# Kernel tuning notes

Hardware: AMD Instinct MI355X
Metric: run time of the kernel (lower is better)

## Reference

```python
import jax, jax.numpy as jnp
import numpy as np

N_HEADS, D_MODEL, DK, DV = 16, 1024, 64, 64
B, S = 4, 2048
NEG = -1000000000.0


def setup_inputs() -> dict:
    key = jax.random.key(0)
    ks = jax.random.split(key, 10)
    inp = {
        "q": jax.random.normal(ks[0], (B, S, D_MODEL), jnp.float32),
        "k": jax.random.normal(ks[1], (B, S, D_MODEL), jnp.float32),
        "v": jax.random.normal(ks[2], (B, S, D_MODEL), jnp.float32),
        "padding_mask": jax.random.randint(ks[3], (B, 1, S), 0, 2, jnp.int32),
        # linear params (torch Linear: y = x @ W.T + b); store as [in, out]
        "w_q": jax.random.normal(ks[4], (D_MODEL, N_HEADS * DK), jnp.float32) * 0.02,
        "b_q": jnp.zeros((N_HEADS * DK,), jnp.float32),
        "w_k": jax.random.normal(ks[5], (D_MODEL, N_HEADS * DK), jnp.float32) * 0.02,
        "b_k": jnp.zeros((N_HEADS * DK,), jnp.float32),
        "w_v": jax.random.normal(ks[6], (D_MODEL, N_HEADS * DV), jnp.float32) * 0.02,
        "b_v": jnp.zeros((N_HEADS * DV,), jnp.float32),
    }
    return inp


def reference(q, k, v, padding_mask, w_q, b_q, w_k, b_k, w_v, b_v):
    residual = q
    # project and split heads: [B, H, S, dk]
    qh = (q @ w_q + b_q).reshape(B, S, N_HEADS, DK).transpose(0, 2, 1, 3)
    kh = (k @ w_k + b_k).reshape(B, S, N_HEADS, DK).transpose(0, 2, 1, 3)
    vh = (v @ w_v + b_v).reshape(B, S, N_HEADS, DV).transpose(0, 2, 1, 3)
    # NB: original code DIVIDES by factor = dk**-0.5, i.e. multiplies by sqrt(dk)
    scores = jnp.einsum("bhqd,bhkd->bhqk", qh, kh) / (DK ** -0.5)
    mask = padding_mask[:, None, :, :]  # [B,1,1,S] broadcasts over heads/queries
    scores = jnp.where(mask == 0, NEG, scores)
    attn = jax.nn.softmax(scores, axis=-1)  # dropout = identity (eval)
    ctx = jnp.einsum("bhqk,bhkd->bhqd", attn, vh)
    ctx = ctx.transpose(0, 2, 1, 3).reshape(B, S, N_HEADS * DV)
    return ctx + residual
```

## Files before the change

kernel.cpp:

```cpp
#include <hip/hip_runtime.h>
#include <hip/hip_fp16.h>

#define BB 4
#define SS 2048
#define HH 16
#define DKK 64
#define DMODEL 1024

typedef __attribute__((ext_vector_type(8))) _Float16 half8;
typedef __attribute__((ext_vector_type(4))) _Float16 half4;
typedef __attribute__((ext_vector_type(2))) __fp16 fp16x2;
typedef __attribute__((ext_vector_type(4))) float floatx4;

#define MFMA16(a, b, c) __builtin_amdgcn_mfma_f32_16x16x32_f16(a, b, c, 0, 0, 0)

#define SCL2 11.5415603336f

__device__ __forceinline__ void gload_lds16(const _Float16* g, _Float16* l) {
    __builtin_amdgcn_global_load_lds(
        (const __attribute__((address_space(1))) void*)g,
        (__attribute__((address_space(3))) void*)l, 16, 0, 0);
}

__device__ __forceinline__
void convert_x_body(const float* __restrict__ src, _Float16* __restrict__ dst,
                    int bidx)
{
    size_t base = ((size_t)bidx * 256 + threadIdx.x) * 8;
    int m = (int)(base >> 10);
    int kk = (int)(base & 1023);
    float4 a = *(const float4*)(src + base);
    float4 b = *(const float4*)(src + base + 4);
    half8 h;
    h[0] = (_Float16)a.x; h[1] = (_Float16)a.y; h[2] = (_Float16)a.z; h[3] = (_Float16)a.w;
    h[4] = (_Float16)b.x; h[5] = (_Float16)b.y; h[6] = (_Float16)b.z; h[7] = (_Float16)b.w;
    int kd = kk ^ ((m & 7) << 3);
    *(half8*)(dst + ((size_t)m << 10) + kd) = h;
}

__device__ __forceinline__
void convert_wt_body(const float* __restrict__ W, _Float16* __restrict__ WT,
                     int bidx)
{
    __shared__ __attribute__((aligned(16))) _Float16 T[64][72];
    int kt = (bidx >> 4) << 6;
    int nt = (bidx & 15) << 6;
    int tid = threadIdx.x;
    #pragma unroll
    for (int p = 0; p < 4; p++) {
        int lin = tid + p * 256;
        int row = lin >> 4;
        int c4 = (lin & 15) << 2;
        float4 vv = *(const float4*)(W + (size_t)(kt + row) * DMODEL + nt + c4);
        T[c4 + 0][row] = (_Float16)vv.x;
        T[c4 + 1][row] = (_Float16)vv.y;
        T[c4 + 2][row] = (_Float16)vv.z;
        T[c4 + 3][row] = (_Float16)vv.w;
    }
    __syncthreads();
    #pragma unroll
    for (int p = 0; p < 2; p++) {
        int lin = tid + p * 256;
        int nl = lin >> 3;
        int u = lin & 7;
        half8 h = *(const half8*)&T[nl][u * 8];
        int n = nt + nl;
        int kd = kt + ((u ^ (n & 7)) << 3);
        *(half8*)(WT + (size_t)n * DMODEL + kd) = h;
    }
}

__global__ __launch_bounds__(256)
void convert_x(const float* __restrict__ q, const float* __restrict__ k,
               const float* __restrict__ v, _Float16* __restrict__ xq,
               _Float16* __restrict__ xk, _Float16* __restrict__ xv)
{
    int z = blockIdx.y;
    convert_x_body(z == 0 ? q : z == 1 ? k : v,
                   z == 0 ? xq : z == 1 ? xk : xv, blockIdx.x);
}

__global__ __launch_bounds__(256)
void convert_wt(const float* __restrict__ wq, const float* __restrict__ wk,
                const float* __restrict__ wv, _Float16* __restrict__ tq,
                _Float16* __restrict__ tk, _Float16* __restrict__ tv)
{
    int z = blockIdx.y;
    convert_wt_body(z == 0 ? wq : z == 1 ? wk : wv,
                    z == 0 ? tq : z == 1 ? tk : tv, blockIdx.x);
}

__global__ __launch_bounds__(256)
void convert_all(const float* __restrict__ q, const float* __restrict__ k,
                 const float* __restrict__ v, const float* __restrict__ wq,
                 const float* __restrict__ wk, const float* __restrict__ wv,
                 _Float16* __restrict__ xq, _Float16* __restrict__ xk,
                 _Float16* __restrict__ xv, _Float16* __restrict__ tq,
                 _Float16* __restrict__ tk, _Float16* __restrict__ tv)
{
    int y = blockIdx.y;
    if (y < 3) {
        convert_x_body(y == 0 ? q : y == 1 ? k : v,
                       y == 0 ? xq : y == 1 ? xk : xv, blockIdx.x);
    } else {
        if (blockIdx.x >= 768) return;
        int z = blockIdx.x >> 8;
        convert_wt_body(z == 0 ? wq : z == 1 ? wk : wv,
                        z == 0 ? tq : z == 1 ? tk : tv, blockIdx.x & 255);
    }
}

template <int VMODE, int SWZ>
__device__ __forceinline__
void proj_body(const _Float16* __restrict__ X, const _Float16* __restrict__ WT,
               const float* __restrict__ bias, _Float16* __restrict__ out,
               int bidx, float scl)
{
    __shared__ __attribute__((aligned(16))) _Float16 As[128 * 64];
    __shared__ __attribute__((aligned(16))) _Float16 Bs[128 * 64];
    const int tid = threadIdx.x;
    const int wave = tid >> 6, lane = tid & 63, quad = lane >> 4, l16 = lane & 15;
    const int wm = wave >> 1, wn = wave & 1;
    const int m0 = ((bidx & 7) | ((bidx >> 6) << 3)) << 7;
    const int n0 = ((bidx >> 3) & 7) << 7;
    const int lrow = lane >> 3;
    const int lcol = (lane & 7) << 3;

    floatx4 acc[4][4] = {};

    for (int k0 = 0; k0 < DMODEL; k0 += 64) {
        __syncthreads();
        #pragma unroll
        for (int c = 0; c < 4; c++) {
            int row = c * 32 + wave * 8;
            gload_lds16(X + (size_t)(m0 + row + lrow) * DMODEL + k0 + lcol,
                        As + (size_t)row * 64);
            gload_lds16(WT + (size_t)(n0 + row + lrow) * DMODEL + k0 + lcol,
                        Bs + (size_t)row * 64);
        }
        __syncthreads();
        #pragma unroll
        for (int ks = 0; ks < 2; ks++) {
            int ccol = ((ks * 4 + quad) ^ (l16 & 7)) << 3;
            half8 af[4], bf[4];
            #pragma unroll
            for (int i = 0; i < 4; i++)
                af[i] = *(const half8*)(As + (wm * 64 + i * 16 + l16) * 64 + ccol);
            #pragma unroll
            for (int j = 0; j < 4; j++)
                bf[j] = *(const half8*)(Bs + (wn * 64 + j * 16 + l16) * 64 + ccol);
            #pragma unroll
            for (int i = 0; i < 4; i++)
                #pragma unroll
                for (int j = 0; j < 4; j++)
                    acc[i][j] = VMODE ? MFMA16(bf[j], af[i], acc[i][j])
                                      : MFMA16(af[i], bf[j], acc[i][j]);
        }
    }

    if (VMODE == 0) {
        #pragma unroll
        for (int j = 0; j < 4; j++) {
            int ng = n0 + wn * 64 + j * 16 + l16;
            int h = ng >> 6, d = ng & 63;
            float bv = bias[ng];
            #pragma unroll
            for (int i = 0; i < 4; i++)
                #pragma unroll
                for (int r = 0; r < 4; r++) {
                    int mg = m0 + wm * 64 + i * 16 + quad * 4 + r;
                    int bb = mg >> 11, s = mg & 2047;
                    int dd = SWZ ? ((((d >> 3) ^ (s & 7)) << 3) | (d & 7)) : d;
                    out[(((size_t)bb * HH + h) * SS + s) * DKK + dd] =
                        (_Float16)((acc[i][j][r] + bv) * scl);
                }
        }
    } else {
        #pragma unroll
        for (int j = 0; j < 4; j++)
            #pragma unroll
            for (int r = 0; r < 4; r++) {
                int ng = n0 + wn * 64 + j * 16 + quad * 4 + r;
                int h = ng >> 6, d = ng & 63;
                float bv = bias[ng];
                #pragma unroll
                for (int i = 0; i < 4; i++) {
                    int mg = m0 + wm * 64 + i * 16 + l16;
                    int bb = mg >> 11, s = mg & 2047;
                    int ss2 = SWZ ? (s ^ ((d & 7) << 3)) : s;
                    out[(((size_t)bb * HH + h) * DKK + d) * SS + ss2] =
                        (_Float16)((acc[i][j][r] + bv) * scl);
                }
            }
    }
}

template <int VMODE, int SWZ>
__global__ __launch_bounds__(256)
void proj128(const _Float16* __restrict__ X, const _Float16* __restrict__ WT,
             const float* __restrict__ bias, _Float16* __restrict__ out, float scl)
{
    proj_body<VMODE, SWZ>(X, WT, bias, out, blockIdx.x, scl);
}

__global__ __launch_bounds__(256)
void proj_all(const _Float16* __restrict__ Xq, const _Float16* __restrict__ Xk,
              const _Float16* __restrict__ Xv, const _Float16* __restrict__ WTq,
              const _Float16* __restrict__ WTk, const _Float16* __restrict__ WTv,
              const float* __restrict__ bq, const float* __restrict__ bk,
              const float* __restrict__ bv, _Float16* __restrict__ Qh,
              _Float16* __restrict__ Kh, _Float16* __restrict__ VTh)
{
    int z = blockIdx.y;
    if (z == 0)      proj_body<0, 0>(Xq, WTq, bq, Qh, blockIdx.x, SCL2);
    else if (z == 1) proj_body<0, 1>(Xk, WTk, bk, Kh, blockIdx.x, 1.0f);
    else             proj_body<1, 1>(Xv, WTv, bv, VTh, blockIdx.x, 1.0f);
}

__global__ __launch_bounds__(256)
void flash3(const _Float16* __restrict__ Qw, const _Float16* __restrict__ Kw,
            const _Float16* __restrict__ VTw, const int* __restrict__ mask,
            const float* __restrict__ resid, float* __restrict__ out)
{
    __shared__ float Bias[SS];
    __shared__ __attribute__((aligned(16))) _Float16 Plds[4][2][16][64];
    __shared__ __attribute__((aligned(16))) _Float16 Ks[2][4096];
    __shared__ __attribute__((aligned(16))) _Float16 Vs[2][4096];

    const int tid = threadIdx.x;
    const int wave = tid >> 6, lane = tid & 63, quad = lane >> 4, l16 = lane & 15;
    const int bx = blockIdx.x;
    const int xcd = bx & 7;
    const int jj = bx >> 3;
    const int bh = ((jj >> 4) << 3) | xcd;
    const int qt = jj & 15;
    const int b = bh >> 4;
    const int h = bh & 15;
    const int qbase = qt * 128 + wave * 32;
    const int sw = l16 & 7;

    const _Float16* Kbase = Kw + (size_t)bh * SS * DKK;
    const _Float16* Vbase = VTw + (size_t)bh * DKK * SS;

    half8 qf[2][2];
    #pragma unroll
    for (int mt = 0; mt < 2; mt++) {
        const _Float16* Qp = Qw + ((size_t)bh * SS + qbase + mt * 16 + l16) * DKK;
        qf[mt][0] = *(const half8*)(Qp + quad * 8);
        qf[mt][1] = *(const half8*)(Qp + 32 + quad * 8);
    }

    #pragma unroll
    for (int c = 0; c < 2; c++) {
        int chunk = wave * 2 + c;
        gload_lds16(Kbase + chunk * 512 + lane * 8, &Ks[0][chunk * 512]);
        gload_lds16(Vbase + (size_t)(chunk * 8 + (lane >> 3)) * SS + (lane & 7) * 8,
                    &Vs[0][chunk * 512]);
    }

    const int* mk = mask + b * SS;
    for (int i = tid; i < SS; i += 256)
        Bias[i] = mk[i] ? 0.f : -1.0e9f;
    asm volatile("s_waitcnt lgkmcnt(0)" ::: "memory");
    __builtin_amdgcn_s_barrier();

    float mrow[2] = {-3.0e38f, -3.0e38f};
    float lrow[2] = {0.f, 0.f};
    floatx4 oacc[2][4] = {};

    for (int kt = 0; kt < SS / 64; kt++) {
        const int cur = kt & 1;
        const _Float16* Kl = Ks[cur];
        const _Float16* Vl = Vs[cur];
        const int kb = kt << 6;

        if (kt < SS / 64 - 1) {
            const int kb1 = kb + 64;
            #pragma unroll
            for (int c = 0; c < 2; c++) {
                int chunk = wave * 2 + c;
                gload_lds16(Kbase + (size_t)kb1 * DKK + chunk * 512 + lane * 8,
                            &Ks[cur ^ 1][chunk * 512]);
                gload_lds16(Vbase + (size_t)(chunk * 8 + (lane >> 3)) * SS + kb1
                                + (lane & 7) * 8,
                            &Vs[cur ^ 1][chunk * 512]);
            }
            asm volatile("s_waitcnt vmcnt(4)" ::: "memory");
        } else {
            asm volatile("s_waitcnt vmcnt(0)" ::: "memory");
        }
        __builtin_amdgcn_s_barrier();

        floatx4 sacc[2][4];
        #pragma unroll
        for (int k2 = 0; k2 < 4; k2++) {
            float4 bv = *(const float4*)&Bias[kb + k2 * 16 + quad * 4];
            floatx4 bi = {bv.x, bv.y, bv.z, bv.w};
            sacc[0][k2] = bi;
            sacc[1][k2] = bi;
        }

        half8 kf[2][4];
        #pragma unroll
        for (int ks = 0; ks < 2; ks++)
            #pragma unroll
            for (int k2 = 0; k2 < 4; k2++)
                kf[ks][k2] = *(const half8*)(Kl + (k2 * 16 + l16) * 64
                                + (((ks * 4 + quad) ^ sw) << 3));

        #pragma unroll
        for (int mt = 0; mt < 2; mt++)
            #pragma unroll
            for (int ks = 0; ks < 2; ks++)
                #pragma unroll
                for (int k2 = 0; k2 < 4; k2++)
                    sacc[mt][k2] = MFMA16(kf[ks][k2], qf[mt][ks], sacc[mt][k2]);

        half8 vf[2][4];
        #pragma unroll
        for (int ks = 0; ks < 2; ks++)
            #pragma unroll
            for (int dt = 0; dt < 4; dt++)
                vf[ks][dt] = *(const half8*)(Vl + (dt * 16 + l16) * 64
                                + (((ks * 4 + quad) ^ sw) << 3));

        #pragma unroll
        for (int mt = 0; mt < 2; mt++) {
            floatx4* S = sacc[mt];

            float t4[4];
            #pragma unroll
            for (int k2 = 0; k2 < 4; k2++)
                t4[k2] = fmaxf(fmaxf(S[k2][0], S[k2][1]),
                               fmaxf(S[k2][2], S[k2][3]));
            float t = fmaxf(fmaxf(t4[0], t4[1]), fmaxf(t4[2], t4[3]));
            t = fmaxf(t, __shfl_xor(t, 16, 64));
            t = fmaxf(t, __shfl_xor(t, 32, 64));

            float mn = fmaxf(mrow[mt], t);
            float al = exp2f(mrow[mt] - mn);
            mrow[mt] = mn;

            float ss[4];
            #pragma unroll
            for (int k2 = 0; k2 < 4; k2++) {
                #pragma unroll
                for (int r = 0; r < 4; r++)
                    S[k2][r] = exp2f(S[k2][r] - mn);
                union { fp16x2 h2[2]; half4 h4; } u;
                u.h2[0] = __builtin_amdgcn_cvt_pkrtz(S[k2][0], S[k2][1]);
                u.h2[1] = __builtin_amdgcn_cvt_pkrtz(S[k2][2], S[k2][3]);
                int cbw = ((((k2 << 1) | (quad >> 1)) ^ sw) << 3) | ((quad & 1) << 2);
                *(half4*)&Plds[wave][mt][l16][cbw] = u.h4;
                ss[k2] = (S[k2][0] + S[k2][1]) + (S[k2][2] + S[k2][3]);
            }
            float ps = (ss[0] + ss[1]) + (ss[2] + ss[3]);
            ps += __shfl_xor(ps, 16, 64);
            ps += __shfl_xor(ps, 32, 64);
            lrow[mt] = lrow[mt] * al + ps;

            #pragma unroll
            for (int dt = 0; dt < 4; dt++)
                oacc[mt][dt] *= al;

            #pragma unroll
            for (int ks = 0; ks < 2; ks++) {
                half8 pf = *(const half8*)
                    &Plds[wave][mt][l16][((ks * 4 + quad) ^ sw) << 3];
                #pragma unroll
                for (int dt = 0; dt < 4; dt++)
                    oacc[mt][dt] = MFMA16(vf[ks][dt], pf, oacc[mt][dt]);
            }
        }
        __builtin_amdgcn_s_barrier();
    }

    #pragma unroll
    for (int mt = 0; mt < 2; mt++) {
        float rl = 1.0f / lrow[mt];
        int s = qbase + mt * 16 + l16;
        size_t rowoff = ((size_t)b * SS + s) * DMODEL + h * DKK;
        #pragma unroll
        for (int dt = 0; dt < 4; dt++) {
            size_t gi = rowoff + dt * 16 + quad * 4;
            float4 rv = *(const float4*)&resid[gi];
            float4 ov;
            ov.x = oacc[mt][dt][0] * rl + rv.x;
            ov.y = oacc[mt][dt][1] * rl + rv.y;
            ov.z = oacc[mt][dt][2] * rl + rv.z;
            ov.w = oacc[mt][dt][3] * rl + rv.w;
            *(float4*)&out[gi] = ov;
        }
    }
}

extern "C" void kernel_launch(void* const* d_in, const int* in_sizes, int n_in,
                              void* d_out, int out_size, void* d_ws, size_t ws_size,
                              hipStream_t stream)
{
    const float* q    = (const float*)d_in[0];
    const float* k    = (const float*)d_in[1];
    const float* v    = (const float*)d_in[2];
    const int*   mask = (const int*)d_in[3];
    const float* wq   = (const float*)d_in[4];
    const float* bq   = (const float*)d_in[5];
    const float* wk   = (const float*)d_in[6];
    const float* bk   = (const float*)d_in[7];
    const float* wv   = (const float*)d_in[8];
    const float* bv   = (const float*)d_in[9];
    float* out = (float*)d_out;

    const size_t TENS = (size_t)BB * SS * HH * DKK;
    const size_t WSZ  = (size_t)DMODEL * DMODEL;
    _Float16* base = (_Float16*)d_ws;

    bool big = ws_size >= (6 * TENS + 3 * WSZ) * sizeof(_Float16);
    _Float16 *Xq, *Xk, *Xv, *Qh, *Kh, *VTh, *WTq;
    if (big) {
        Xq = base;            Xk = base + TENS;     Xv = base + 2 * TENS;
        Qh = base + 3 * TENS; Kh = base + 4 * TENS; VTh = base + 5 * TENS;
        WTq = base + 6 * TENS;
    } else {
        Xq = base;            Xk = base + TENS;     Xv = base + 2 * TENS;
        Qh = base + 3 * TENS; Kh = Xq;              VTh = Xk;
        WTq = base + 4 * TENS;
    }
    _Float16* WTk = WTq + WSZ;
    _Float16* WTv = WTk + WSZ;

    if (big) {
        hipLaunchKernelGGL(convert_all, dim3(4096, 4), dim3(256), 0, stream,
                           q, k, v, wq, wk, wv, Xq, Xk, Xv, WTq, WTk, WTv);
        hipLaunchKernelGGL(proj_all, dim3(512, 3), dim3(256), 0, stream,
                           Xq, Xk, Xv, WTq, WTk, WTv, bq, bk, bv, Qh, Kh, VTh);
    } else {
        hipLaunchKernelGGL(convert_x, dim3(4096, 3), dim3(256), 0, stream,
                           q, k, v, Xq, Xk, Xv);
        hipLaunchKernelGGL(convert_wt, dim3(256, 3), dim3(256), 0, stream,
                           wq, wk, wv, WTq, WTk, WTv);
        hipLaunchKernelGGL((proj128<0, 0>), dim3(512), dim3(256), 0, stream, Xq, WTq, bq, Qh, SCL2);
        hipLaunchKernelGGL((proj128<0, 1>), dim3(512), dim3(256), 0, stream, Xk, WTk, bk, Kh, 1.0f);
        hipLaunchKernelGGL((proj128<1, 1>), dim3(512), dim3(256), 0, stream, Xv, WTv, bv, VTh, 1.0f);
    }
    hipLaunchKernelGGL(flash3, dim3(BB * HH * (SS / 128)), dim3(256), 0, stream,
                       Qh, Kh, VTh, mask, q, out);
}
```

Baseline: 515.8 us.

## Load V fragments directly from global memory and shrink flash kernel LDS footprint

The attention kernel stops staging V tiles in shared memory. Each wave now reads its V fragments straight from global memory into registers, and the V projection drops the LDS swizzle layout to match. The mask bias is stored as fp16 and the P staging buffer is cut to one tile per wave, which lowers LDS use and may raise occupancy. Scheduling priority is raised around the MFMA blocks. The trade-off is that V reads now go through L2 with less latency hiding, and the masked value becomes -30000 in fp16 instead of -1e9.

```diff
diff --git a/kernel.cpp b/kernel.cpp
--- a/kernel.cpp
+++ b/kernel.cpp
@@ -214,7 +214,7 @@
     int z = blockIdx.y;
     if (z == 0)      proj_body<0, 0>(Xq, WTq, bq, Qh, blockIdx.x, SCL2);
     else if (z == 1) proj_body<0, 1>(Xk, WTk, bk, Kh, blockIdx.x, 1.0f);
-    else             proj_body<1, 1>(Xv, WTv, bv, VTh, blockIdx.x, 1.0f);
+    else             proj_body<1, 0>(Xv, WTv, bv, VTh, blockIdx.x, 1.0f);
 }
 
 __global__ __launch_bounds__(256)
@@ -222,10 +222,9 @@
             const _Float16* __restrict__ VTw, const int* __restrict__ mask,
             const float* __restrict__ resid, float* __restrict__ out)
 {
-    __shared__ float Bias[SS];
-    __shared__ __attribute__((aligned(16))) _Float16 Plds[4][2][16][64];
+    __shared__ _Float16 BiasH[SS];
+    __shared__ __attribute__((aligned(16))) _Float16 Plds[4][16][64];
     __shared__ __attribute__((aligned(16))) _Float16 Ks[2][4096];
-    __shared__ __attribute__((aligned(16))) _Float16 Vs[2][4096];
 
     const int tid = threadIdx.x;
     const int wave = tid >> 6, lane = tid & 63, quad = lane >> 4, l16 = lane & 15;
@@ -254,13 +253,11 @@
     for (int c = 0; c < 2; c++) {
         int chunk = wave * 2 + c;
         gload_lds16(Kbase + chunk * 512 + lane * 8, &Ks[0][chunk * 512]);
-        gload_lds16(Vbase + (size_t)(chunk * 8 + (lane >> 3)) * SS + (lane & 7) * 8,
-                    &Vs[0][chunk * 512]);
     }
 
     const int* mk = mask + b * SS;
     for (int i = tid; i < SS; i += 256)
-        Bias[i] = mk[i] ? 0.f : -1.0e9f;
+        BiasH[i] = mk[i] ? (_Float16)0.0f : (_Float16)-30000.0f;
     asm volatile("s_waitcnt lgkmcnt(0)" ::: "memory");
     __builtin_amdgcn_s_barrier();
 
@@ -271,7 +268,6 @@
     for (int kt = 0; kt < SS / 64; kt++) {
         const int cur = kt & 1;
         const _Float16* Kl = Ks[cur];
-        const _Float16* Vl = Vs[cur];
         const int kb = kt << 6;
 
         if (kt < SS / 64 - 1) {
@@ -281,11 +277,8 @@
                 int chunk = wave * 2 + c;
                 gload_lds16(Kbase + (size_t)kb1 * DKK + chunk * 512 + lane * 8,
                             &Ks[cur ^ 1][chunk * 512]);
-                gload_lds16(Vbase + (size_t)(chunk * 8 + (lane >> 3)) * SS + kb1
-                                + (lane & 7) * 8,
-                            &Vs[cur ^ 1][chunk * 512]);
             }
-            asm volatile("s_waitcnt vmcnt(4)" ::: "memory");
+            asm volatile("s_waitcnt vmcnt(2)" ::: "memory");
         } else {
             asm volatile("s_waitcnt vmcnt(0)" ::: "memory");
         }
@@ -294,35 +287,35 @@
         floatx4 sacc[2][4];
         #pragma unroll
         for (int k2 = 0; k2 < 4; k2++) {
-            float4 bv = *(const float4*)&Bias[kb + k2 * 16 + quad * 4];
-            floatx4 bi = {bv.x, bv.y, bv.z, bv.w};
+            half4 bh4 = *(const half4*)&BiasH[kb + k2 * 16 + quad * 4];
+            floatx4 bi = {(float)bh4[0], (float)bh4[1], (float)bh4[2], (float)bh4[3]};
             sacc[0][k2] = bi;
             sacc[1][k2] = bi;
         }
 
-        half8 kf[2][4];
+        __builtin_amdgcn_s_setprio(1);
+        #pragma unroll
+        for (int ks = 0; ks < 2; ks++) {
+            half8 kf[4];
+            #pragma unroll
+            for (int k2 = 0; k2 < 4; k2++)
+                kf[k2] = *(const half8*)(Kl + (k2 * 16 + l16) * 64
+                                + (((ks * 4 + quad) ^ sw) << 3));
+            #pragma unroll
+            for (int mt = 0; mt < 2; mt++)
+                #pragma unroll
+                for (int k2 = 0; k2 < 4; k2++)
+                    sacc[mt][k2] = MFMA16(kf[k2], qf[mt][ks], sacc[mt][k2]);
+        }
+        __builtin_amdgcn_s_setprio(0);
+
+        half8 vf[2][4];
         #pragma unroll
         for (int ks = 0; ks < 2; ks++)
             #pragma unroll
-            for (int k2 = 0; k2 < 4; k2++)
-                kf[ks][k2] = *(const half8*)(Kl + (k2 * 16 + l16) * 64
-                                + (((ks * 4 + quad) ^ sw) << 3));
-
-        #pragma unroll
-        for (int mt = 0; mt < 2; mt++)
-            #pragma unroll
-            for (int ks = 0; ks < 2; ks++)
-                #pragma unroll
-                for (int k2 = 0; k2 < 4; k2++)
-                    sacc[mt][k2] = MFMA16(kf[ks][k2], qf[mt][ks], sacc[mt][k2]);
-
-        half8 vf[2][4];
-        #pragma unroll
-        for (int ks = 0; ks < 2; ks++)
-            #pragma unroll
             for (int dt = 0; dt < 4; dt++)
-                vf[ks][dt] = *(const half8*)(Vl + (dt * 16 + l16) * 64
-                                + (((ks * 4 + quad) ^ sw) << 3));
+                vf[ks][dt] = *(const half8*)(Vbase
+                    + (size_t)(dt * 16 + l16) * SS + kb + ks * 32 + quad * 8);
 
         #pragma unroll
         for (int mt = 0; mt < 2; mt++) {
@@ -351,7 +344,7 @@
                 u.h2[0] = __builtin_amdgcn_cvt_pkrtz(S[k2][0], S[k2][1]);
                 u.h2[1] = __builtin_amdgcn_cvt_pkrtz(S[k2][2], S[k2][3]);
                 int cbw = ((((k2 << 1) | (quad >> 1)) ^ sw) << 3) | ((quad & 1) << 2);
-                *(half4*)&Plds[wave][mt][l16][cbw] = u.h4;
+                *(half4*)&Plds[wave][l16][cbw] = u.h4;
                 ss[k2] = (S[k2][0] + S[k2][1]) + (S[k2][2] + S[k2][3]);
             }
             float ps = (ss[0] + ss[1]) + (ss[2] + ss[3]);
@@ -363,14 +356,16 @@
             for (int dt = 0; dt < 4; dt++)
                 oacc[mt][dt] *= al;
 
+            __builtin_amdgcn_s_setprio(1);
             #pragma unroll
             for (int ks = 0; ks < 2; ks++) {
                 half8 pf = *(const half8*)
-                    &Plds[wave][mt][l16][((ks * 4 + quad) ^ sw) << 3];
+                    &Plds[wave][l16][((ks * 4 + quad) ^ sw) << 3];
                 #pragma unroll
                 for (int dt = 0; dt < 4; dt++)
                     oacc[mt][dt] = MFMA16(vf[ks][dt], pf, oacc[mt][dt]);
             }
+            __builtin_amdgcn_s_setprio(0);
         }
         __builtin_amdgcn_s_barrier();
     }
@@ -440,7 +435,7 @@
                            wq, wk, wv, WTq, WTk, WTv);
         hipLaunchKernelGGL((proj128<0, 0>), dim3(512), dim3(256), 0, stream, Xq, WTq, bq, Qh, SCL2);
         hipLaunchKernelGGL((proj128<0, 1>), dim3(512), dim3(256), 0, stream, Xk, WTk, bk, Kh, 1.0f);
-        hipLaunchKernelGGL((proj128<1, 1>), dim3(512), dim3(256), 0, stream, Xv, WTv, bv, VTh, 1.0f);
+        hipLaunchKernelGGL((proj128<1, 0>), dim3(512), dim3(256), 0, stream, Xv, WTv, bv, VTh, 1.0f);
     }
     hipLaunchKernelGGL(flash3, dim3(BB * HH * (SS / 128)), dim3(256), 0, stream,
                        Qh, Kh, VTh, mask, q, out);
```

Measured after the change: 469.2 us. -9.0%, faster.
